# Kernel optimization log

Hardware: AMD Instinct MI355X
Metric: run time of the kernel (lower is better)

Reference implementation:

```python
import jax, jax.numpy as jnp
import numpy as np

TWO_PI = 2.0 * np.pi
EPS = 1e-12  # torch F.normalize eps


def setup_inputs() -> dict:
    key = jax.random.key(0)
    ks = jax.random.split(key, 12)
    B, NS, G = 16, 128, 20000
    P, S, E, T = 200, 128, 128, 50
    return {
        "x_genes": jax.random.normal(ks[0], (B, NS, G), jnp.float32),
        "tissue_idx": jax.random.randint(ks[1], (B, NS), 0, T, jnp.int32),
        "pathway_idx": jax.random.randint(ks[2], (P, S), 0, G, jnp.int32),
        "W_proj": jax.random.normal(ks[3], (P, E, S), jnp.float32) * (1.0 / np.sqrt(S)),
        "b_proj": jax.random.normal(ks[4], (P, E), jnp.float32) * 0.02,
        "tissue_table": jax.random.normal(ks[5], (T, E), jnp.float32),
        "W1": jax.random.normal(ks[6], (E, 32), jnp.float32) * (1.0 / np.sqrt(E)),
        "b1": jax.random.normal(ks[7], (32,), jnp.float32) * 0.02,
        "W2": jax.random.normal(ks[8], (32, 2), jnp.float32) * (1.0 / np.sqrt(32)),
        "b2": jax.random.normal(ks[9], (2,), jnp.float32) * 0.02,
        "Wdec": jax.random.normal(ks[10], (2, G), jnp.float32) * (1.0 / np.sqrt(2.0)),
        "bdec": jax.random.normal(ks[11], (G,), jnp.float32) * 0.02,
    }


def _l2norm(v):
    n = jnp.sqrt(jnp.sum(v * v, axis=-1, keepdims=True))
    return v / jnp.maximum(n, EPS)


def reference(x_genes, tissue_idx, pathway_idx, W_proj, b_proj, tissue_table,
              W1, b1, W2, b2, Wdec, bdec):
    B, NS, G = x_genes.shape
    x = x_genes.reshape(-1, G)            # [N, G], N = B*NS
    t = tissue_idx.reshape(-1)            # [N]

    # Pathway tokenizer: gather gene subsets + per-pathway linear (grouped GEMM)
    xg = x[:, pathway_idx]                # [N, P, S]
    H = jax.nn.relu(jnp.einsum('nps,pes->npe', xg, W_proj) + b_proj)  # [N, P, E]

    # Single-query attention with tissue embedding as query
    Q = tissue_table[t]                   # [N, E]
    scale = 1.0 / np.sqrt(H.shape[-1])
    scores = jnp.einsum('ne,npe->np', Q, H) * scale   # [N, P]
    attn = jax.nn.softmax(scores, axis=-1)
    context = jnp.einsum('np,npe->ne', attn, H)       # [N, E]

    # to_latent MLP (dropout=0 / eval)
    h = jax.nn.relu(context @ W1 + b1)
    pc = h @ W2 + b2                      # [N, 2]
    pcn = _l2norm(pc)
    ang = jnp.remainder(jnp.arctan2(pcn[:, 1], pcn[:, 0]) + TWO_PI, TWO_PI)

    # decode + normalize
    rec = _l2norm(pcn @ Wdec + bdec)      # [N, G]

    return (pcn.reshape(B, NS, 2), ang.reshape(B, NS), rec.reshape(B, NS, G))
```

## Files before the change

### kernel.cpp

```cpp
#include <hip/hip_runtime.h>
#include <cmath>

#define GG 20000
#define NN 2048
#define PP 200
#define SS 128
#define EE 128
#define TN 128
#define TPP 8
#define NOCT 25

typedef __bf16 bf16x8 __attribute__((ext_vector_type(8)));
typedef float f32x16 __attribute__((ext_vector_type(16)));
typedef unsigned short u16x8 __attribute__((ext_vector_type(8)));

__device__ __align__(16) unsigned g_xTi[(size_t)GG * NN];
__device__ __align__(16) unsigned short g_Wsw[(size_t)PP * 32768];
__device__ float g_ctxp[(size_t)NN * NOCT * EE];
__device__ float g_mT[NOCT * NN];
__device__ float g_lT[NOCT * NN];

__device__ __forceinline__ unsigned short f2bf(float f) {
  unsigned u = __builtin_bit_cast(unsigned, f);
  return (unsigned short)((u + 0x7FFFu + ((u >> 16) & 1u)) >> 16);
}
__device__ __forceinline__ float bf2f(unsigned short h) {
  return __builtin_bit_cast(float, (unsigned)h << 16);
}
__device__ __forceinline__ unsigned packhl(float f) {
  unsigned short h = f2bf(f);
  unsigned short l = f2bf(f - bf2f(h));
  return (unsigned)h | ((unsigned)l << 16);
}

__global__ __launch_bounds__(256) void transpose_convert_kernel(
    const float* __restrict__ x)
{
  __shared__ float tile[64][65];
  const int g0 = blockIdx.x * 64;
  const int n0 = blockIdx.y * 64;
  const int t = threadIdx.x;
  {
    const int gq = t & 15, nl4 = t >> 4;
    #pragma unroll
    for (int k = 0; k < 4; ++k) {
      int nl = nl4 + 16 * k;
      int g = g0 + gq * 4;
      if (g + 3 < GG) {
        float4 v = *(const float4*)&x[(size_t)(n0 + nl) * GG + g];
        tile[gq * 4 + 0][nl] = v.x;
        tile[gq * 4 + 1][nl] = v.y;
        tile[gq * 4 + 2][nl] = v.z;
        tile[gq * 4 + 3][nl] = v.w;
      }
    }
  }
  __syncthreads();
  {
    const int nq = t & 15, gl4 = t >> 4;
    #pragma unroll
    for (int k = 0; k < 4; ++k) {
      int gl = gl4 + 16 * k;
      int g = g0 + gl;
      if (g < GG) {
        uint4 v;
        v.x = packhl(tile[gl][nq * 4 + 0]);
        v.y = packhl(tile[gl][nq * 4 + 1]);
        v.z = packhl(tile[gl][nq * 4 + 2]);
        v.w = packhl(tile[gl][nq * 4 + 3]);
        *(uint4*)&g_xTi[(size_t)g * NN + n0 + nq * 4] = v;
      }
    }
  }
}

__global__ __launch_bounds__(256) void wconvert_kernel(const float* __restrict__ Wp)
{
  unsigned v = blockIdx.x * 256 + threadIdx.x;
  const int si = v & 7;
  const int slp = (v >> 3) & 7;
  const int e = (v >> 6) & 127;
  const int ch = (v >> 13) & 1;
  const int p = v >> 14;
  const int slot = slp ^ (e & 7);
  const int s = ch * 64 + slot * 8 + si;
  float f = Wp[((size_t)p * EE + e) * SS + s];
  unsigned short h = f2bf(f);
  unsigned short l = f2bf(f - bf2f(h));
  size_t base = (size_t)(p * 2 + ch) * 16384 + e * 64 + slp * 8 + si;
  g_Wsw[base] = h;
  g_Wsw[base + 8192] = l;
}

__device__ __forceinline__ void load16(unsigned* xr, const int* sidx_lds,
                                       int sbase, int kh, int ncol) {
  #pragma unroll
  for (int ks2 = 0; ks2 < 2; ++ks2)
    #pragma unroll
    for (int j = 0; j < 8; ++j) {
      int s = (sbase + ks2) * 16 + kh * 8 + j;
      xr[ks2 * 8 + j] = g_xTi[(size_t)sidx_lds[s] * NN + ncol];
    }
}

__device__ __forceinline__ void compute2ks(const unsigned short* wb,
                                           const unsigned* xr, f32x16 (&acc)[4],
                                           int ksbase, int nl, int kh) {
  #pragma unroll
  for (int ks2 = 0; ks2 < 2; ++ks2) {
    const int ks = ksbase + ks2;
    const unsigned short* wAh = wb + (ks >> 2) * 16384;
    const unsigned short* wAl = wAh + 8192;
    u16x8 bhu, blu;
    #pragma unroll
    for (int j = 0; j < 8; ++j) {
      unsigned v = xr[ks2 * 8 + j];
      bhu[j] = (unsigned short)(v & 0xffffu);
      blu[j] = (unsigned short)(v >> 16);
    }
    bf16x8 bh = __builtin_bit_cast(bf16x8, bhu);
    bf16x8 bl = __builtin_bit_cast(bf16x8, blu);
    #pragma unroll
    for (int et = 0; et < 4; ++et) {
      const int e = et * 32 + nl;
      const int slp = ((ks & 3) * 2 + kh) ^ (e & 7);
      bf16x8 ah = __builtin_bit_cast(bf16x8, *(const uint4*)(wAh + e * 64 + slp * 8));
      bf16x8 al = __builtin_bit_cast(bf16x8, *(const uint4*)(wAl + e * 64 + slp * 8));
      acc[et] = __builtin_amdgcn_mfma_f32_32x32x16_bf16(ah, bh, acc[et], 0, 0, 0);
      acc[et] = __builtin_amdgcn_mfma_f32_32x32x16_bf16(ah, bl, acc[et], 0, 0, 0);
      acc[et] = __builtin_amdgcn_mfma_f32_32x32x16_bf16(al, bh, acc[et], 0, 0, 0);
    }
  }
}

__device__ __forceinline__ void pathway_body(
    int p, unsigned short* wbuf, int* sidx, float* sbp,
    const int* __restrict__ pidx, const float* __restrict__ bp,
    const float* __restrict__ tt, int tid_n,
    int t, int w, int ln, int nl, int kh, int ncol,
    f32x16 (&h)[4], float& s_out)
{
  __syncthreads();
  if (t < 128) sidx[t] = pidx[p * SS + t];
  else         sbp[t - 128] = bp[p * EE + (t - 128)];
  {
    const unsigned short* src = g_Wsw + (size_t)p * 32768 + w * 8192 + ln * 8;
    unsigned short* dst = wbuf + w * 8192;
    #pragma unroll
    for (int j = 0; j < 16; ++j) {
      __builtin_amdgcn_global_load_lds(
          (const __attribute__((address_space(1))) unsigned int*)(src + j * 512),
          (__attribute__((address_space(3))) unsigned int*)(dst + j * 512), 16, 0, 0);
    }
  }
  __syncthreads();

  #pragma unroll
  for (int et = 0; et < 4; ++et)
    #pragma unroll
    for (int r = 0; r < 16; ++r) h[et][r] = 0.f;

  unsigned xa[16], xb[16];
  load16(xa, sidx, 0, kh, ncol);
  load16(xb, sidx, 2, kh, ncol);
  compute2ks(wbuf, xa, h, 0, nl, kh);
  load16(xa, sidx, 4, kh, ncol);
  compute2ks(wbuf, xb, h, 2, nl, kh);
  load16(xb, sidx, 6, kh, ncol);
  compute2ks(wbuf, xa, h, 4, nl, kh);
  compute2ks(wbuf, xb, h, 6, nl, kh);

  const float4* qp = (const float4*)(tt + (size_t)tid_n * EE);
  float scr = 0.f;
  #pragma unroll
  for (int et = 0; et < 4; ++et)
    #pragma unroll
    for (int rq = 0; rq < 4; ++rq) {
      int e0 = et * 32 + rq * 8 + kh * 4;
      float4 q4 = qp[e0 >> 2];
      float4 b4 = *(const float4*)&sbp[e0];
      float h0 = fmaxf(h[et][rq * 4 + 0] + b4.x, 0.f);
      float h1 = fmaxf(h[et][rq * 4 + 1] + b4.y, 0.f);
      float h2 = fmaxf(h[et][rq * 4 + 2] + b4.z, 0.f);
      float h3 = fmaxf(h[et][rq * 4 + 3] + b4.w, 0.f);
      h[et][rq * 4 + 0] = h0; h[et][rq * 4 + 1] = h1;
      h[et][rq * 4 + 2] = h2; h[et][rq * 4 + 3] = h3;
      scr += h0 * q4.x + h1 * q4.y + h2 * q4.z + h3 * q4.w;
    }
  scr += __shfl_xor(scr, 32);
  s_out = scr * 0.08838834764831845f;
}

__global__ __launch_bounds__(256, 2) void proj_mfma_kernel(
    const int* __restrict__ tidx, const int* __restrict__ pidx,
    const float* __restrict__ bp, const float* __restrict__ tt)
{
  __shared__ __align__(16) unsigned short wbuf[32768];
  __shared__ int sidx[SS];
  __shared__ float sbp[EE];

  const int t = threadIdx.x;
  const int w = t >> 6;
  const int ln = t & 63;
  const int nl = ln & 31;
  const int kh = ln >> 5;
  const int n0 = blockIdx.x * TN;
  const int oct = blockIdx.y;
  const int ncol = n0 + w * 32 + nl;
  const int tid_n = tidx[ncol];

  f32x16 ctx[4];
  #pragma unroll
  for (int et = 0; et < 4; ++et)
    #pragma unroll
    for (int r = 0; r < 16; ++r) ctx[et][r] = 0.f;
  float m_r = -1e30f, l_r = 0.f;

  f32x16 h[4];
  float s;
  for (int pp = 0; pp < TPP; ++pp) {
    pathway_body(oct * TPP + pp, wbuf, sidx, sbp, pidx, bp, tt, tid_n,
                 t, w, ln, nl, kh, ncol, h, s);
    const float mn = fmaxf(m_r, s);
    const float f = expf(m_r - mn);
    const float wg = expf(s - mn);
    l_r = l_r * f + wg;
    m_r = mn;
    #pragma unroll
    for (int et = 0; et < 4; ++et)
      #pragma unroll
      for (int r = 0; r < 16; ++r)
        ctx[et][r] = ctx[et][r] * f + wg * h[et][r];
  }

  __syncthreads();
  float* tb = ((float*)wbuf) + w * (32 * 128);
  #pragma unroll
  for (int et = 0; et < 4; ++et)
    #pragma unroll
    for (int rq = 0; rq < 4; ++rq) {
      int slot = et * 8 + rq * 2 + kh;
      float4 v = make_float4(ctx[et][rq * 4 + 0], ctx[et][rq * 4 + 1],
                             ctx[et][rq * 4 + 2], ctx[et][rq * 4 + 3]);
      *(float4*)&tb[nl * 128 + ((slot ^ nl) << 2)] = v;
    }
  __syncthreads();
  {
    const int rrow = ln >> 1, eh = (ln & 1) * 16;
    const int nn = n0 + w * 32 + rrow;
    float* dst = g_ctxp + ((size_t)nn * NOCT + oct) * EE + eh * 4;
    const float* srcrow = tb + rrow * 128;
    #pragma unroll
    for (int k = 0; k < 16; ++k) {
      int slot = eh + k;
      *(float4*)&dst[k * 4] = *(const float4*)&srcrow[(slot ^ rrow) << 2];
    }
  }
  if (ln < 32) {
    g_mT[oct * NN + ncol] = m_r;
    g_lT[oct * NN + ncol] = l_r;
  }
}

__global__ __launch_bounds__(256) void combine_rec_kernel(
    const float* __restrict__ W1, const float* __restrict__ b1,
    const float* __restrict__ W2, const float* __restrict__ b2,
    const float* __restrict__ Wdec, const float* __restrict__ bdec,
    float* __restrict__ out)
{
  const int n = blockIdx.x;
  const int t = threadIdx.x;
  __shared__ float ws[NOCT];
  __shared__ float ctx2[2][EE];
  __shared__ float r1[4], r2[4];
  __shared__ float hsh[32];
  __shared__ float qsh[2];
  __shared__ float red[4];

  float mv = (t < NOCT) ? g_mT[t * NN + n] : -1e30f;
  float lv = (t < NOCT) ? g_lT[t * NN + n] : 0.f;
  float M = mv;
  #pragma unroll
  for (int off = 32; off >= 1; off >>= 1) M = fmaxf(M, __shfl_xor(M, off));
  if ((t & 63) == 0) r1[t >> 6] = M;
  __syncthreads();
  M = fmaxf(fmaxf(r1[0], r1[1]), fmaxf(r1[2], r1[3]));
  float wv = (t < NOCT) ? expf(mv - M) : 0.f;
  if (t < NOCT) ws[t] = wv;
  float Lp = wv * lv;
  #pragma unroll
  for (int off = 32; off >= 1; off >>= 1) Lp += __shfl_xor(Lp, off);
  if ((t & 63) == 0) r2[t >> 6] = Lp;
  __syncthreads();
  const float L = r2[0] + r2[1] + r2[2] + r2[3];

  {
    const int e = t & 127, hf = t >> 7;
    const int sA = hf ? 13 : 0, sB = hf ? NOCT : 13;
    const float* base = g_ctxp + ((size_t)n * NOCT + sA) * EE + e;
    float c = 0.f;
    for (int s = sA; s < sB; ++s) c += ws[s] * base[(size_t)(s - sA) * EE];
    ctx2[hf][e] = c;
  }
  __syncthreads();
  const float invL = 1.f / L;
  if (t < 32) {
    float h = 0.f;
    for (int e = 0; e < EE; ++e) h += (ctx2[0][e] + ctx2[1][e]) * W1[e * 32 + t];
    hsh[t] = fmaxf(h * invL + b1[t], 0.f);
  }
  __syncthreads();
  if (t == 0) {
    float p0 = b2[0], p1 = b2[1];
    #pragma unroll
    for (int k = 0; k < 32; ++k) { p0 += hsh[k] * W2[k * 2]; p1 += hsh[k] * W2[k * 2 + 1]; }
    float inv = 1.f / fmaxf(sqrtf(p0 * p0 + p1 * p1), 1e-12f);
    float q0 = p0 * inv, q1 = p1 * inv;
    const float PI2 = 6.2831853071795864769f;
    float ang = atan2f(q1, q0) + PI2;
    if (ang >= PI2) ang -= PI2;
    out[n * 2 + 0] = q0;
    out[n * 2 + 1] = q1;
    out[2 * NN + n] = ang;
    qsh[0] = q0; qsh[1] = q1;
  }
  __syncthreads();
  const float q0 = qsh[0], q1 = qsh[1];

  float ss = 0.f;
  for (int i = t; i < GG / 4; i += 256) {
    float4 w0 = *(const float4*)&Wdec[i * 4];
    float4 w1 = *(const float4*)&Wdec[GG + i * 4];
    float4 bd = *(const float4*)&bdec[i * 4];
    float v0 = q0 * w0.x + q1 * w1.x + bd.x;
    float v1 = q0 * w0.y + q1 * w1.y + bd.y;
    float v2 = q0 * w0.z + q1 * w1.z + bd.z;
    float v3 = q0 * w0.w + q1 * w1.w + bd.w;
    ss += v0 * v0 + v1 * v1 + v2 * v2 + v3 * v3;
  }
  #pragma unroll
  for (int off = 32; off >= 1; off >>= 1) ss += __shfl_xor(ss, off);
  if ((t & 63) == 0) red[t >> 6] = ss;
  __syncthreads();
  const float inv = 1.f / fmaxf(sqrtf(red[0] + red[1] + red[2] + red[3]), 1e-12f);

  float* orec = out + 3 * NN + (size_t)n * GG;
  for (int i = t; i < GG / 4; i += 256) {
    float4 w0 = *(const float4*)&Wdec[i * 4];
    float4 w1 = *(const float4*)&Wdec[GG + i * 4];
    float4 bd = *(const float4*)&bdec[i * 4];
    float4 o;
    o.x = (q0 * w0.x + q1 * w1.x + bd.x) * inv;
    o.y = (q0 * w0.y + q1 * w1.y + bd.y) * inv;
    o.z = (q0 * w0.z + q1 * w1.z + bd.z) * inv;
    o.w = (q0 * w0.w + q1 * w1.w + bd.w) * inv;
    *(float4*)&orec[i * 4] = o;
  }
}

extern "C" void kernel_launch(void* const* d_in, const int* in_sizes, int n_in,
                              void* d_out, int out_size, void* d_ws, size_t ws_size,
                              hipStream_t stream) {
  (void)in_sizes; (void)n_in; (void)out_size; (void)d_ws; (void)ws_size;
  const float* x    = (const float*)d_in[0];
  const int*   tidx = (const int*)  d_in[1];
  const int*   pidx = (const int*)  d_in[2];
  const float* Wp   = (const float*)d_in[3];
  const float* bp   = (const float*)d_in[4];
  const float* tt   = (const float*)d_in[5];
  const float* W1   = (const float*)d_in[6];
  const float* b1   = (const float*)d_in[7];
  const float* W2   = (const float*)d_in[8];
  const float* b2   = (const float*)d_in[9];
  const float* Wdec = (const float*)d_in[10];
  const float* bdec = (const float*)d_in[11];
  float* out = (float*)d_out;

  dim3 gridT((GG + 63) / 64, NN / 64, 1);
  transpose_convert_kernel<<<gridT, 256, 0, stream>>>(x);
  wconvert_kernel<<<(PP * 16384) / 256, 256, 0, stream>>>(Wp);

  dim3 gridA(NN / TN, NOCT, 1);
  proj_mfma_kernel<<<gridA, 256, 0, stream>>>(tidx, pidx, bp, tt);

  combine_rec_kernel<<<NN, 256, 0, stream>>>(W1, b1, W2, b2, Wdec, bdec, out);
}
```

Before: 286.2 us.

## Widen projection blocks to 512 threads, halve pathways per block, split decode kernel

The projection kernel now runs 256 columns per block with 8 waves and handles 4 pathways per block, giving 50 pathway groups instead of 25. The context store is staged through shared memory in two phases so it fits the same 64 KB buffer. The combine step now reduces over 50 partials and saves q0, q1 and the norm to a small global array. A separate kernel then writes the reconstruction, using two blocks per row. The goal is more parallelism and better occupancy, but the 512-thread, 4-blocks-per-CU launch bound sharply limits registers for large accumulators and may cause spills; the extra launch and partial traffic also add cost.

```diff
diff --git a/kernel.cpp b/kernel.cpp
--- a/kernel.cpp
+++ b/kernel.cpp
@@ -6,9 +6,9 @@
 #define PP 200
 #define SS 128
 #define EE 128
-#define TN 128
-#define TPP 8
-#define NOCT 25
+#define TN 256
+#define TPP 4
+#define NOCT 50
 
 typedef __bf16 bf16x8 __attribute__((ext_vector_type(8)));
 typedef float f32x16 __attribute__((ext_vector_type(16)));
@@ -19,6 +19,7 @@
 __device__ float g_ctxp[(size_t)NN * NOCT * EE];
 __device__ float g_mT[NOCT * NN];
 __device__ float g_lT[NOCT * NN];
+__device__ float g_q[NN * 4];
 
 __device__ __forceinline__ unsigned short f2bf(float f) {
   unsigned u = __builtin_bit_cast(unsigned, f);
@@ -142,12 +143,12 @@
 {
   __syncthreads();
   if (t < 128) sidx[t] = pidx[p * SS + t];
-  else         sbp[t - 128] = bp[p * EE + (t - 128)];
+  else if (t < 256) sbp[t - 128] = bp[p * EE + (t - 128)];
   {
-    const unsigned short* src = g_Wsw + (size_t)p * 32768 + w * 8192 + ln * 8;
-    unsigned short* dst = wbuf + w * 8192;
-    #pragma unroll
-    for (int j = 0; j < 16; ++j) {
+    const unsigned short* src = g_Wsw + (size_t)p * 32768 + w * 4096 + ln * 8;
+    unsigned short* dst = wbuf + w * 4096;
+    #pragma unroll
+    for (int j = 0; j < 8; ++j) {
       __builtin_amdgcn_global_load_lds(
           (const __attribute__((address_space(1))) unsigned int*)(src + j * 512),
           (__attribute__((address_space(3))) unsigned int*)(dst + j * 512), 16, 0, 0);
@@ -191,7 +192,7 @@
   s_out = scr * 0.08838834764831845f;
 }
 
-__global__ __launch_bounds__(256, 2) void proj_mfma_kernel(
+__global__ __launch_bounds__(512, 4) void proj_mfma_kernel(
     const int* __restrict__ tidx, const int* __restrict__ pidx,
     const float* __restrict__ bp, const float* __restrict__ tt)
 {
@@ -234,27 +235,35 @@
   }
 
   __syncthreads();
-  float* tb = ((float*)wbuf) + w * (32 * 128);
-  #pragma unroll
-  for (int et = 0; et < 4; ++et)
-    #pragma unroll
-    for (int rq = 0; rq < 4; ++rq) {
-      int slot = et * 8 + rq * 2 + kh;
-      float4 v = make_float4(ctx[et][rq * 4 + 0], ctx[et][rq * 4 + 1],
-                             ctx[et][rq * 4 + 2], ctx[et][rq * 4 + 3]);
-      *(float4*)&tb[nl * 128 + ((slot ^ nl) << 2)] = v;
-    }
-  __syncthreads();
-  {
-    const int rrow = ln >> 1, eh = (ln & 1) * 16;
-    const int nn = n0 + w * 32 + rrow;
-    float* dst = g_ctxp + ((size_t)nn * NOCT + oct) * EE + eh * 4;
-    const float* srcrow = tb + rrow * 128;
-    #pragma unroll
-    for (int k = 0; k < 16; ++k) {
-      int slot = eh + k;
-      *(float4*)&dst[k * 4] = *(const float4*)&srcrow[(slot ^ rrow) << 2];
-    }
+  float* tbase = (float*)wbuf;
+  #pragma unroll
+  for (int ph = 0; ph < 2; ++ph) {
+    if ((w >> 2) == ph) {
+      float* tb = tbase + (w & 3) * 4096;
+      #pragma unroll
+      for (int et = 0; et < 4; ++et)
+        #pragma unroll
+        for (int rq = 0; rq < 4; ++rq) {
+          int slot = et * 8 + rq * 2 + kh;
+          float4 v = make_float4(ctx[et][rq * 4 + 0], ctx[et][rq * 4 + 1],
+                                 ctx[et][rq * 4 + 2], ctx[et][rq * 4 + 3]);
+          *(float4*)&tb[nl * 128 + ((slot ^ nl) << 2)] = v;
+        }
+    }
+    __syncthreads();
+    if ((w >> 2) == ph) {
+      float* tb = tbase + (w & 3) * 4096;
+      const int rrow = ln >> 1, eh = (ln & 1) * 16;
+      const int nn = n0 + w * 32 + rrow;
+      float* dst = g_ctxp + ((size_t)nn * NOCT + oct) * EE + eh * 4;
+      const float* srcrow = tb + rrow * 128;
+      #pragma unroll
+      for (int k = 0; k < 16; ++k) {
+        int slot = eh + k;
+        *(float4*)&dst[k * 4] = *(const float4*)&srcrow[(slot ^ rrow) << 2];
+      }
+    }
+    __syncthreads();
   }
   if (ln < 32) {
     g_mT[oct * NN + ncol] = m_r;
@@ -262,7 +271,7 @@
   }
 }
 
-__global__ __launch_bounds__(256) void combine_rec_kernel(
+__global__ __launch_bounds__(256) void combine_kernel(
     const float* __restrict__ W1, const float* __restrict__ b1,
     const float* __restrict__ W2, const float* __restrict__ b2,
     const float* __restrict__ Wdec, const float* __restrict__ bdec,
@@ -296,10 +305,11 @@
 
   {
     const int e = t & 127, hf = t >> 7;
-    const int sA = hf ? 13 : 0, sB = hf ? NOCT : 13;
+    const int sA = hf * 25;
     const float* base = g_ctxp + ((size_t)n * NOCT + sA) * EE + e;
     float c = 0.f;
-    for (int s = sA; s < sB; ++s) c += ws[s] * base[(size_t)(s - sA) * EE];
+    #pragma unroll 5
+    for (int s = 0; s < 25; ++s) c += ws[sA + s] * base[(size_t)s * EE];
     ctx2[hf][e] = c;
   }
   __syncthreads();
@@ -342,18 +352,38 @@
   for (int off = 32; off >= 1; off >>= 1) ss += __shfl_xor(ss, off);
   if ((t & 63) == 0) red[t >> 6] = ss;
   __syncthreads();
-  const float inv = 1.f / fmaxf(sqrtf(red[0] + red[1] + red[2] + red[3]), 1e-12f);
-
-  float* orec = out + 3 * NN + (size_t)n * GG;
-  for (int i = t; i < GG / 4; i += 256) {
-    float4 w0 = *(const float4*)&Wdec[i * 4];
-    float4 w1 = *(const float4*)&Wdec[GG + i * 4];
-    float4 bd = *(const float4*)&bdec[i * 4];
+  if (t == 0) {
+    const float inv = 1.f / fmaxf(sqrtf(red[0] + red[1] + red[2] + red[3]), 1e-12f);
+    g_q[n * 4 + 0] = q0;
+    g_q[n * 4 + 1] = q1;
+    g_q[n * 4 + 2] = inv;
+  }
+}
+
+__global__ __launch_bounds__(256) void rec_write_kernel(
+    const float* __restrict__ Wdec, const float* __restrict__ bdec,
+    float* __restrict__ out)
+{
+  const int bid = blockIdx.x;
+  const int n = bid >> 1;
+  const int half = bid & 1;
+  const float q0 = g_q[n * 4 + 0];
+  const float q1 = g_q[n * 4 + 1];
+  const float inv = g_q[n * 4 + 2];
+  const int base = half * (GG / 2);
+  const float* wd0 = Wdec + base;
+  const float* wd1 = Wdec + GG + base;
+  const float* bd = bdec + base;
+  float* orec = out + 3 * NN + (size_t)n * GG + base;
+  for (int i = threadIdx.x; i < GG / 8; i += 256) {
+    float4 w0 = *(const float4*)&wd0[i * 4];
+    float4 w1 = *(const float4*)&wd1[i * 4];
+    float4 b4 = *(const float4*)&bd[i * 4];
     float4 o;
-    o.x = (q0 * w0.x + q1 * w1.x + bd.x) * inv;
-    o.y = (q0 * w0.y + q1 * w1.y + bd.y) * inv;
-    o.z = (q0 * w0.z + q1 * w1.z + bd.z) * inv;
-    o.w = (q0 * w0.w + q1 * w1.w + bd.w) * inv;
+    o.x = (q0 * w0.x + q1 * w1.x + b4.x) * inv;
+    o.y = (q0 * w0.y + q1 * w1.y + b4.y) * inv;
+    o.z = (q0 * w0.z + q1 * w1.z + b4.z) * inv;
+    o.w = (q0 * w0.w + q1 * w1.w + b4.w) * inv;
     *(float4*)&orec[i * 4] = o;
   }
 }
@@ -381,7 +411,8 @@
   wconvert_kernel<<<(PP * 16384) / 256, 256, 0, stream>>>(Wp);
 
   dim3 gridA(NN / TN, NOCT, 1);
-  proj_mfma_kernel<<<gridA, 256, 0, stream>>>(tidx, pidx, bp, tt);
-
-  combine_rec_kernel<<<NN, 256, 0, stream>>>(W1, b1, W2, b2, Wdec, bdec, out);
-}
+  proj_mfma_kernel<<<gridA, 512, 0, stream>>>(tidx, pidx, bp, tt);
+
+  combine_kernel<<<NN, 256, 0, stream>>>(W1, b1, W2, b2, Wdec, bdec, out);
+  rec_write_kernel<<<NN * 2, 256, 0, stream>>>(Wdec, bdec, out);
+}
```

New measurement: 366.0 us. 27.9% more time.
